# Kernel tuning notes

Measured on AMD Instinct MI355X. Metric: run time of the kernel, lower is better.

Reference implementation:

```python
import jax, jax.numpy as jnp
import numpy as np

B_, T_, DX_, DZ_ = 64, 1024, 64, 1024


def setup_inputs() -> dict:
    key = jax.random.key(0)
    k1, k2, k3, k4, k5 = jax.random.split(key, 5)
    x = jax.random.normal(k1, (B_, T_, DX_), dtype=jnp.float32)
    # obs_model weight (nn.Linear(d_z, d_x).weight): shape (d_x, d_z)
    Bw = jax.random.normal(k2, (DX_, DZ_), dtype=jnp.float32) / np.sqrt(DZ_).astype(np.float32)
    # nn.RNN params (uniform +-1/sqrt(d_z) like torch init)
    bound = 1.0 / np.sqrt(DZ_).astype(np.float32)
    W_hh = jax.random.uniform(k3, (DZ_, DZ_), dtype=jnp.float32, minval=-bound, maxval=bound)
    b_ih = jax.random.uniform(k4, (DZ_,), dtype=jnp.float32, minval=-bound, maxval=bound)
    b_hh = jax.random.uniform(k5, (DZ_,), dtype=jnp.float32, minval=-bound, maxval=bound)
    return {"x": x, "Bw": Bw, "W_hh": W_hh, "b_ih": b_ih, "b_hh": b_hh, "n": 64}


def reference(x, Bw, W_hh, b_ih, b_hh, n):
    # x: (b, T, d_x); Bw: (d_x, d_z); W_hh: (d_z, d_z)
    b, T, dx = x.shape
    pinvB = jnp.linalg.pinv(Bw)                      # (d_z, d_x)
    # candidate reset states z_t = (pinv(B) @ x[:, t].T).T for all t
    zx = jnp.einsum('btx,zx->btz', x, pinvB)         # (b, T, d_z)
    # reset at t == 0 (initial h) and every t % n == 0 (t != 0 case coincides
    # with t == 0 where h is already zx[:, 0], so a single mask is exact)
    reset = (jnp.arange(T) % n) == 0                 # (T,) bool
    bias = b_ih + b_hh                               # input is zero: W_ih @ 0 drops out

    def step(h, inputs):
        m, zr = inputs                               # m: scalar bool, zr: (b, d_z)
        h_in = jnp.where(m, zr, h)
        out = jnp.tanh(h_in @ W_hh.T + bias)         # vanilla tanh RNN cell, zero input
        return out, out

    zr_seq = jnp.swapaxes(zx, 0, 1)                  # (T, b, d_z)
    _, zs = jax.lax.scan(step, zx[:, 0], (reset, zr_seq))
    return jnp.swapaxes(zs, 0, 1)                    # (b, T, d_z)
```

## Files before the change

### kernel.cpp

```cpp
#include <hip/hip_runtime.h>
#include <cstdint>
#include <cstddef>

typedef __attribute__((ext_vector_type(8))) __bf16 bf16x8;
typedef __attribute__((ext_vector_type(4))) float  f32x4;

static_assert(sizeof(bf16x8) == 16, "bf16x8 must be 16B");

__device__ __forceinline__ float fast_tanh(float x) {
    float e = __expf(2.0f * x);
    return 1.0f - 2.0f * __builtin_amdgcn_rcpf(e + 1.0f);
}

__device__ __forceinline__ bf16x8 load_h(const __bf16* p) {
    union { bf16x8 v; unsigned long long q[2]; } u;
    unsigned long long* qp = (unsigned long long*)p;
    u.q[0] = __hip_atomic_load(qp, __ATOMIC_RELAXED, __HIP_MEMORY_SCOPE_AGENT);
    u.q[1] = __hip_atomic_load(qp + 1, __ATOMIC_RELAXED, __HIP_MEMORY_SCOPE_AGENT);
    return u.v;
}

__global__ void k_bias(const float* __restrict__ b_ih, const float* __restrict__ b_hh,
                       float* __restrict__ bias, int* __restrict__ cnt) {
    int i = blockIdx.x * 256 + threadIdx.x;
    bias[i] = b_ih[i] + b_hh[i];
    if (blockIdx.x == 0) cnt[threadIdx.x] = 0;
}

__global__ void k_shufw(const float* __restrict__ W, __bf16* __restrict__ Ws) {
    int id = blockIdx.x * 256 + threadIdx.x;
    int t = id >> 11;
    int c = (id >> 6) & 31;
    int L = id & 63;
    const float* src = W + (size_t)(t * 16 + (L & 15)) * 1024 + c * 32 + (L >> 4) * 8;
    __bf16* dst = Ws + (size_t)id * 8;
#pragma unroll
    for (int j = 0; j < 8; ++j) dst[j] = (__bf16)src[j];
}

__global__ void k_gram(const float* __restrict__ Bw, float* __restrict__ M) {
    int i = blockIdx.x;
    int j = threadIdx.x >> 2;
    int q = threadIdx.x & 3;
    const float4* a = (const float4*)(Bw + (size_t)i * 1024) + q * 64;
    const float4* b = (const float4*)(Bw + (size_t)j * 1024) + q * 64;
    float acc = 0.f;
#pragma unroll 8
    for (int t = 0; t < 64; ++t) {
        float4 av = a[t], bv = b[t];
        acc += av.x * bv.x + av.y * bv.y + av.z * bv.z + av.w * bv.w;
    }
    acc += __shfl_xor(acc, 1);
    acc += __shfl_xor(acc, 2);
    if (q == 0) M[i * 64 + j] = acc;
}

__global__ __launch_bounds__(1024) void k_newton(const float* __restrict__ M,
                                                 float* __restrict__ Minv) {
    __shared__ float Mm[4096];
    __shared__ float X[4096];
    __shared__ float Tt[4096];
    const int tid = threadIdx.x;
    const int i = tid & 63;
    const int w = tid >> 6;
    for (int p = tid; p < 4096; p += 1024) {
        Mm[p] = M[p];
        int r = p >> 6, c2 = p & 63;
        X[p] = (r == c2) ? 0.941f : 0.0f;
    }
    __syncthreads();
    for (int it = 0; it < 6; ++it) {
        float r[4] = {0.f, 0.f, 0.f, 0.f};
        for (int kk = 0; kk < 64; ++kk) {
            float mv = Mm[(kk << 6) + i];
            float4 x4 = *(const float4*)&X[(kk << 6) + (w << 2)];
            r[0] += mv * x4.x; r[1] += mv * x4.y; r[2] += mv * x4.z; r[3] += mv * x4.w;
        }
#pragma unroll
        for (int jj = 0; jj < 4; ++jj) Tt[(((w << 2) + jj) << 6) + i] = r[jj];
        __syncthreads();
        float r2[4];
#pragma unroll
        for (int jj = 0; jj < 4; ++jj) r2[jj] = 2.f * X[(((w << 2) + jj) << 6) + i];
        for (int kq = 0; kq < 16; ++kq) {
            float xv0 = X[((kq * 4 + 0) << 6) + i];
            float xv1 = X[((kq * 4 + 1) << 6) + i];
            float xv2 = X[((kq * 4 + 2) << 6) + i];
            float xv3 = X[((kq * 4 + 3) << 6) + i];
#pragma unroll
            for (int jj = 0; jj < 4; ++jj) {
                float4 t4 = *(const float4*)&Tt[(((w << 2) + jj) << 6) + (kq << 2)];
                r2[jj] -= xv0 * t4.x + xv1 * t4.y + xv2 * t4.z + xv3 * t4.w;
            }
        }
        __syncthreads();
#pragma unroll
        for (int jj = 0; jj < 4; ++jj) X[(((w << 2) + jj) << 6) + i] = r2[jj];
        __syncthreads();
    }
    for (int p = tid; p < 4096; p += 1024) Minv[p] = X[p];
}

__global__ void k_t1(const float* __restrict__ x, const float* __restrict__ Minv,
                     float* __restrict__ T1) {
    int id = blockIdx.x * 256 + threadIdx.x;
    int r = id >> 6, xp = id & 63;
    const float* xr = x + ((size_t)(r >> 4) * 1024 + (size_t)(r & 15) * 64) * 64;
    const float* mr = Minv + (size_t)xp * 64;
    float acc = 0.f;
    for (int t = 0; t < 64; ++t) acc += xr[t] * mr[t];
    T1[id] = acc;
}

__global__ void k_h0(const float* __restrict__ T1, const float* __restrict__ Bw,
                     __bf16* __restrict__ H0) {
    int r = blockIdx.y;
    int z = blockIdx.x * 256 + threadIdx.x;
    const float* t1 = T1 + (size_t)r * 64;
    float acc = 0.f;
    for (int xp = 0; xp < 64; ++xp) acc += t1[xp] * Bw[(size_t)xp * 1024 + z];
    H0[(size_t)r * 1024 + z] = (__bf16)acc;
}

__global__ __launch_bounds__(256) void k_step(
    const __bf16* __restrict__ Hin, const __bf16* __restrict__ Ws,
    const float* __restrict__ bias, __bf16* __restrict__ Hout,
    float* __restrict__ out, int kstep) {
    const int tid = threadIdx.x;
    const int w = tid >> 6;
    const int lane = tid & 63;
    const int row = lane & 15;
    const int quad = lane >> 4;
    const int bm = blockIdx.x, bn = blockIdx.y;

    const __bf16* Arow = Hin + (size_t)(bm * 64 + w * 16 + row) * 1024 + quad * 8;
    const __bf16* B0 = Ws + ((size_t)((bn * 2 + 0) * 32) * 64 + lane) * 8;
    const __bf16* B1 = Ws + ((size_t)((bn * 2 + 1) * 32) * 64 + lane) * 8;

    f32x4 acc0 = {0.f, 0.f, 0.f, 0.f};
    f32x4 acc1 = {0.f, 0.f, 0.f, 0.f};
#pragma unroll 8
    for (int c = 0; c < 32; ++c) {
        bf16x8 a = *(const bf16x8*)(Arow + c * 32);
        bf16x8 b0 = *(const bf16x8*)(B0 + (size_t)c * 512);
        bf16x8 b1 = *(const bf16x8*)(B1 + (size_t)c * 512);
        acc0 = __builtin_amdgcn_mfma_f32_16x16x32_bf16(a, b0, acc0, 0, 0, 0);
        acc1 = __builtin_amdgcn_mfma_f32_16x16x32_bf16(a, b1, acc1, 0, 0, 0);
    }
#pragma unroll
    for (int nt = 0; nt < 2; ++nt) {
        const f32x4 acc = nt ? acc1 : acc0;
        const int col = bn * 32 + nt * 16 + row;
        const float bv = bias[col];
#pragma unroll
        for (int i = 0; i < 4; ++i) {
            const int m = bm * 64 + w * 16 + quad * 4 + i;
            float v = tanhf(acc[i] + bv);
            const int b_ = m >> 4, s_ = m & 15;
            out[((size_t)b_ * 1024 + (size_t)s_ * 64 + kstep) * 1024 + col] = v;
            Hout[(size_t)m * 1024 + col] = (__bf16)v;
        }
    }
}

__global__ __launch_bounds__(256, 1) void k_persist(
    const __bf16* __restrict__ Ws, const float* __restrict__ bias,
    __bf16* __restrict__ H0, __bf16* __restrict__ H1,
    float* __restrict__ out, int* cnt) {
    __shared__ __bf16 Bs[65536];
    const int tid = threadIdx.x;
    const int bid = blockIdx.x;
    const int bm = bid & 15;
    const int bn = bid >> 4;
    const int lane = tid & 63;
    const int w = tid >> 6;
    const int row = lane & 15, quad = lane >> 4;

    {
        const bf16x8* src = (const bf16x8*)(Ws + ((size_t)bn << 16));
        bf16x8* dst = (bf16x8*)Bs;
#pragma unroll
        for (int it = 0; it < 32; ++it) dst[it * 256 + tid] = src[it * 256 + tid];
    }
    float bv[4];
#pragma unroll
    for (int nt = 0; nt < 4; ++nt) bv[nt] = bias[bn * 64 + nt * 16 + row];
    __syncthreads();

    const size_t aoff = (size_t)(bm * 64 + w * 16 + row) * 1024 + quad * 8;
    int* mycnt = cnt + bm * 16;

    for (int k = 0; k < 64; ++k) {
        const __bf16* Hin = (k & 1) ? H1 : H0;
        __bf16* Hout = (k & 1) ? H0 : H1;
        const __bf16* A = Hin + aoff;
        const bf16x8* Bl = (const bf16x8*)Bs + lane;

        f32x4 acc0 = {0.f, 0.f, 0.f, 0.f};
        f32x4 acc1 = acc0, acc2 = acc0, acc3 = acc0;

        bf16x8 a0 = load_h(A + 0 * 32), a1 = load_h(A + 1 * 32),
               a2 = load_h(A + 2 * 32), a3 = load_h(A + 3 * 32),
               a4 = load_h(A + 4 * 32), a5 = load_h(A + 5 * 32),
               a6 = load_h(A + 6 * 32), a7 = load_h(A + 7 * 32);

#define KSTEP(AA, CC)                                                                     \
        acc0 = __builtin_amdgcn_mfma_f32_16x16x32_bf16(AA, Bl[(0 * 32 + (CC)) * 64], acc0, 0, 0, 0); \
        acc1 = __builtin_amdgcn_mfma_f32_16x16x32_bf16(AA, Bl[(1 * 32 + (CC)) * 64], acc1, 0, 0, 0); \
        acc2 = __builtin_amdgcn_mfma_f32_16x16x32_bf16(AA, Bl[(2 * 32 + (CC)) * 64], acc2, 0, 0, 0); \
        acc3 = __builtin_amdgcn_mfma_f32_16x16x32_bf16(AA, Bl[(3 * 32 + (CC)) * 64], acc3, 0, 0, 0);

        for (int c = 0; c < 24; c += 8) {
            bf16x8 n0 = load_h(A + (c + 8) * 32),  n1 = load_h(A + (c + 9) * 32),
                   n2 = load_h(A + (c + 10) * 32), n3 = load_h(A + (c + 11) * 32),
                   n4 = load_h(A + (c + 12) * 32), n5 = load_h(A + (c + 13) * 32),
                   n6 = load_h(A + (c + 14) * 32), n7 = load_h(A + (c + 15) * 32);
            KSTEP(a0, c + 0) KSTEP(a1, c + 1) KSTEP(a2, c + 2) KSTEP(a3, c + 3)
            KSTEP(a4, c + 4) KSTEP(a5, c + 5) KSTEP(a6, c + 6) KSTEP(a7, c + 7)
            a0 = n0; a1 = n1; a2 = n2; a3 = n3; a4 = n4; a5 = n5; a6 = n6; a7 = n7;
        }
        KSTEP(a0, 24) KSTEP(a1, 25) KSTEP(a2, 26) KSTEP(a3, 27)
        KSTEP(a4, 28) KSTEP(a5, 29) KSTEP(a6, 30) KSTEP(a7, 31)
#undef KSTEP

        const int mbase = bm * 64 + w * 16 + quad * 4;
#pragma unroll
        for (int nt = 0; nt < 4; ++nt) {
            const f32x4 acc = nt == 0 ? acc0 : nt == 1 ? acc1 : nt == 2 ? acc2 : acc3;
            const int col = bn * 64 + nt * 16 + row;
            const float bb = bv[nt];
#pragma unroll
            for (int i2 = 0; i2 < 4; ++i2) {
                const int m = mbase + i2;
                const float v = fast_tanh(acc[i2] + bb);
                const int b_ = m >> 4, s_ = m & 15;
                out[((size_t)b_ * 1024 + (size_t)s_ * 64 + k) * 1024 + col] = v;
                if (k < 63) {
                    union { __bf16 h; unsigned short s; } cv;
                    cv.h = (__bf16)v;
                    __hip_atomic_store((unsigned short*)(Hout + (size_t)m * 1024 + col),
                                       cv.s, __ATOMIC_RELAXED, __HIP_MEMORY_SCOPE_AGENT);
                }
            }
        }

        __syncthreads();
        if (k < 63) {
            if (tid == 0) {
                __hip_atomic_fetch_add(mycnt, 1, __ATOMIC_RELAXED, __HIP_MEMORY_SCOPE_AGENT);
                const int target = (k + 1) * 16;
                while (__hip_atomic_load(mycnt, __ATOMIC_RELAXED, __HIP_MEMORY_SCOPE_AGENT) < target)
                    __builtin_amdgcn_s_sleep(1);
            }
            __syncthreads();
        }
    }
}

extern "C" void kernel_launch(void* const* d_in, const int* in_sizes, int n_in,
                              void* d_out, int out_size, void* d_ws, size_t ws_size,
                              hipStream_t stream) {
    const float* x = (const float*)d_in[0];
    const float* Bw = (const float*)d_in[1];
    const float* W_hh = (const float*)d_in[2];
    const float* b_ih = (const float*)d_in[3];
    const float* b_hh = (const float*)d_in[4];
    float* out = (float*)d_out;
    uint8_t* ws = (uint8_t*)d_ws;

    __bf16* Ws = (__bf16*)(ws);
    __bf16* H0 = (__bf16*)(ws + (2ull << 20));
    __bf16* H1 = (__bf16*)(ws + (4ull << 20));
    float* bias = (float*)(ws + (6ull << 20));
    float* Mg = (float*)(ws + (6ull << 20) + 4096);
    float* Minv = (float*)(ws + (6ull << 20) + 20480);
    float* T1 = (float*)(ws + (6ull << 20) + 36864);
    int* cnt = (int*)(ws + (6ull << 20) + 36864 + 262144);

    hipLaunchKernelGGL(k_bias, dim3(4), dim3(256), 0, stream, b_ih, b_hh, bias, cnt);
    hipLaunchKernelGGL(k_shufw, dim3(512), dim3(256), 0, stream, W_hh, Ws);
    hipLaunchKernelGGL(k_gram, dim3(64), dim3(256), 0, stream, Bw, Mg);
    hipLaunchKernelGGL(k_newton, dim3(1), dim3(1024), 0, stream, Mg, Minv);
    hipLaunchKernelGGL(k_t1, dim3(256), dim3(256), 0, stream, x, Minv, T1);
    hipLaunchKernelGGL(k_h0, dim3(4, 1024), dim3(256), 0, stream, T1, Bw, H0);

    const __bf16* Wsp = Ws;
    const float* biasp = bias;
    __bf16* h0p = H0;
    __bf16* h1p = H1;
    float* outp = out;
    int* cntp = cnt;
    void* kargs[] = {&Wsp, &biasp, &h0p, &h1p, &outp, &cntp};
    hipError_t err = hipLaunchCooperativeKernel((void*)k_persist, dim3(256), dim3(256),
                                                kargs, 0, stream);
    if (err != hipSuccess) {
        __bf16* bufs[2] = {H0, H1};
        for (int k = 0; k < 64; ++k) {
            hipLaunchKernelGGL(k_step, dim3(16, 32), dim3(256), 0, stream,
                               bufs[k & 1], Ws, bias, bufs[(k + 1) & 1], out, k);
        }
    }
}
```

Baseline: 913.6 us.

## Stage persistent-kernel outputs through LDS for vectorized stores after the barrier

The persistent recurrence kernel now writes tanh results into a padded shared-memory tile, then reads them back so each thread owns 16 contiguous columns of one row. The bf16 hidden-state handoff becomes four 64-bit atomic stores instead of scalar 16-bit atomics. The fp32 output is written with nontemporal 16-byte stores issued after the inter-block barrier, so it overlaps the next step instead of delaying the handoff. All 32 A fragments are also loaded up front. This costs an extra LDS round trip and barrier per step, more registers, and 17 KB more shared memory.

```diff
diff --git a/kernel.cpp b/kernel.cpp
--- a/kernel.cpp
+++ b/kernel.cpp
@@ -6,18 +6,11 @@
 typedef __attribute__((ext_vector_type(4))) float  f32x4;
 
 static_assert(sizeof(bf16x8) == 16, "bf16x8 must be 16B");
+static_assert(sizeof(f32x4) == 16, "f32x4 must be 16B");
 
 __device__ __forceinline__ float fast_tanh(float x) {
     float e = __expf(2.0f * x);
     return 1.0f - 2.0f * __builtin_amdgcn_rcpf(e + 1.0f);
-}
-
-__device__ __forceinline__ bf16x8 load_h(const __bf16* p) {
-    union { bf16x8 v; unsigned long long q[2]; } u;
-    unsigned long long* qp = (unsigned long long*)p;
-    u.q[0] = __hip_atomic_load(qp, __ATOMIC_RELAXED, __HIP_MEMORY_SCOPE_AGENT);
-    u.q[1] = __hip_atomic_load(qp + 1, __ATOMIC_RELAXED, __HIP_MEMORY_SCOPE_AGENT);
-    return u.v;
 }
 
 __global__ void k_bias(const float* __restrict__ b_ih, const float* __restrict__ b_hh,
@@ -168,13 +161,13 @@
     __bf16* __restrict__ H0, __bf16* __restrict__ H1,
     float* __restrict__ out, int* cnt) {
     __shared__ __bf16 Bs[65536];
+    __shared__ float oT[64 * 68];
     const int tid = threadIdx.x;
-    const int bid = blockIdx.x;
-    const int bm = bid & 15;
-    const int bn = bid >> 4;
     const int lane = tid & 63;
     const int w = tid >> 6;
     const int row = lane & 15, quad = lane >> 4;
+    const int bm = blockIdx.x & 15;
+    const int bn = blockIdx.x >> 4;
 
     {
         const bf16x8* src = (const bf16x8*)(Ws + ((size_t)bn << 16));
@@ -188,72 +181,90 @@
     __syncthreads();
 
     const size_t aoff = (size_t)(bm * 64 + w * 16 + row) * 1024 + quad * 8;
-    int* mycnt = cnt + bm * 16;
+    int* gcnt = cnt + bm * 16;
+    const bf16x8* Bl = (const bf16x8*)Bs + lane;
+
+    const int tr = tid >> 2;
+    const int tc = (tid & 3) << 4;
+    const int gm = bm * 64 + tr;
+    float* outp = out + ((size_t)(gm >> 4) * 1024 + (size_t)(gm & 15) * 64) * 1024
+                      + (size_t)bn * 64 + tc;
+    const size_t hoff = (size_t)gm * 1024 + (size_t)(bn * 64 + tc);
 
     for (int k = 0; k < 64; ++k) {
         const __bf16* Hin = (k & 1) ? H1 : H0;
         __bf16* Hout = (k & 1) ? H0 : H1;
-        const __bf16* A = Hin + aoff;
-        const bf16x8* Bl = (const bf16x8*)Bs + lane;
+        const unsigned long long* Aq = (const unsigned long long*)(Hin + aoff);
+
+        bf16x8 av[32];
+#pragma unroll
+        for (int c = 0; c < 32; ++c) {
+            union { bf16x8 v; unsigned long long q[2]; } u;
+            u.q[0] = __hip_atomic_load(Aq + c * 8,     __ATOMIC_RELAXED,
+                                       __HIP_MEMORY_SCOPE_AGENT);
+            u.q[1] = __hip_atomic_load(Aq + c * 8 + 1, __ATOMIC_RELAXED,
+                                       __HIP_MEMORY_SCOPE_AGENT);
+            av[c] = u.v;
+        }
 
         f32x4 acc0 = {0.f, 0.f, 0.f, 0.f};
         f32x4 acc1 = acc0, acc2 = acc0, acc3 = acc0;
-
-        bf16x8 a0 = load_h(A + 0 * 32), a1 = load_h(A + 1 * 32),
-               a2 = load_h(A + 2 * 32), a3 = load_h(A + 3 * 32),
-               a4 = load_h(A + 4 * 32), a5 = load_h(A + 5 * 32),
-               a6 = load_h(A + 6 * 32), a7 = load_h(A + 7 * 32);
-
-#define KSTEP(AA, CC)                                                                     \
-        acc0 = __builtin_amdgcn_mfma_f32_16x16x32_bf16(AA, Bl[(0 * 32 + (CC)) * 64], acc0, 0, 0, 0); \
-        acc1 = __builtin_amdgcn_mfma_f32_16x16x32_bf16(AA, Bl[(1 * 32 + (CC)) * 64], acc1, 0, 0, 0); \
-        acc2 = __builtin_amdgcn_mfma_f32_16x16x32_bf16(AA, Bl[(2 * 32 + (CC)) * 64], acc2, 0, 0, 0); \
-        acc3 = __builtin_amdgcn_mfma_f32_16x16x32_bf16(AA, Bl[(3 * 32 + (CC)) * 64], acc3, 0, 0, 0);
-
-        for (int c = 0; c < 24; c += 8) {
-            bf16x8 n0 = load_h(A + (c + 8) * 32),  n1 = load_h(A + (c + 9) * 32),
-                   n2 = load_h(A + (c + 10) * 32), n3 = load_h(A + (c + 11) * 32),
-                   n4 = load_h(A + (c + 12) * 32), n5 = load_h(A + (c + 13) * 32),
-                   n6 = load_h(A + (c + 14) * 32), n7 = load_h(A + (c + 15) * 32);
-            KSTEP(a0, c + 0) KSTEP(a1, c + 1) KSTEP(a2, c + 2) KSTEP(a3, c + 3)
-            KSTEP(a4, c + 4) KSTEP(a5, c + 5) KSTEP(a6, c + 6) KSTEP(a7, c + 7)
-            a0 = n0; a1 = n1; a2 = n2; a3 = n3; a4 = n4; a5 = n5; a6 = n6; a7 = n7;
-        }
-        KSTEP(a0, 24) KSTEP(a1, 25) KSTEP(a2, 26) KSTEP(a3, 27)
-        KSTEP(a4, 28) KSTEP(a5, 29) KSTEP(a6, 30) KSTEP(a7, 31)
-#undef KSTEP
-
-        const int mbase = bm * 64 + w * 16 + quad * 4;
+#pragma unroll
+        for (int c = 0; c < 32; ++c) {
+            acc0 = __builtin_amdgcn_mfma_f32_16x16x32_bf16(av[c], Bl[(0 * 32 + c) * 64], acc0, 0, 0, 0);
+            acc1 = __builtin_amdgcn_mfma_f32_16x16x32_bf16(av[c], Bl[(1 * 32 + c) * 64], acc1, 0, 0, 0);
+            acc2 = __builtin_amdgcn_mfma_f32_16x16x32_bf16(av[c], Bl[(2 * 32 + c) * 64], acc2, 0, 0, 0);
+            acc3 = __builtin_amdgcn_mfma_f32_16x16x32_bf16(av[c], Bl[(3 * 32 + c) * 64], acc3, 0, 0, 0);
+        }
+
 #pragma unroll
         for (int nt = 0; nt < 4; ++nt) {
             const f32x4 acc = nt == 0 ? acc0 : nt == 1 ? acc1 : nt == 2 ? acc2 : acc3;
-            const int col = bn * 64 + nt * 16 + row;
-            const float bb = bv[nt];
 #pragma unroll
             for (int i2 = 0; i2 < 4; ++i2) {
-                const int m = mbase + i2;
-                const float v = fast_tanh(acc[i2] + bb);
-                const int b_ = m >> 4, s_ = m & 15;
-                out[((size_t)b_ * 1024 + (size_t)s_ * 64 + k) * 1024 + col] = v;
-                if (k < 63) {
-                    union { __bf16 h; unsigned short s; } cv;
-                    cv.h = (__bf16)v;
-                    __hip_atomic_store((unsigned short*)(Hout + (size_t)m * 1024 + col),
-                                       cv.s, __ATOMIC_RELAXED, __HIP_MEMORY_SCOPE_AGENT);
-                }
+                const int r = w * 16 + quad * 4 + i2;
+                oT[r * 68 + nt * 16 + row] = fast_tanh(acc[i2] + bv[nt]);
             }
         }
-
+        __syncthreads();
+
+        const f32x4 o0 = *(const f32x4*)&oT[tr * 68 + tc + 0];
+        const f32x4 o1 = *(const f32x4*)&oT[tr * 68 + tc + 4];
+        const f32x4 o2 = *(const f32x4*)&oT[tr * 68 + tc + 8];
+        const f32x4 o3 = *(const f32x4*)&oT[tr * 68 + tc + 12];
+
+        if (k < 63) {
+            union { __bf16 h[16]; unsigned long long q[4]; } hp;
+#pragma unroll
+            for (int j = 0; j < 4; ++j) {
+                hp.h[0 + j] = (__bf16)o0[j];
+                hp.h[4 + j] = (__bf16)o1[j];
+                hp.h[8 + j] = (__bf16)o2[j];
+                hp.h[12 + j] = (__bf16)o3[j];
+            }
+            unsigned long long* hq = (unsigned long long*)(Hout + hoff);
+#pragma unroll
+            for (int j = 0; j < 4; ++j)
+                __hip_atomic_store(hq + j, hp.q[j], __ATOMIC_RELAXED,
+                                   __HIP_MEMORY_SCOPE_AGENT);
+        }
         __syncthreads();
         if (k < 63) {
             if (tid == 0) {
-                __hip_atomic_fetch_add(mycnt, 1, __ATOMIC_RELAXED, __HIP_MEMORY_SCOPE_AGENT);
+                __hip_atomic_fetch_add(gcnt, 1, __ATOMIC_RELAXED,
+                                       __HIP_MEMORY_SCOPE_AGENT);
                 const int target = (k + 1) * 16;
-                while (__hip_atomic_load(mycnt, __ATOMIC_RELAXED, __HIP_MEMORY_SCOPE_AGENT) < target)
+                while (__hip_atomic_load(gcnt, __ATOMIC_RELAXED,
+                                         __HIP_MEMORY_SCOPE_AGENT) < target)
                     __builtin_amdgcn_s_sleep(1);
             }
             __syncthreads();
         }
+        float* op = outp + (size_t)k * 1024;
+        __builtin_nontemporal_store(o0, (f32x4*)(op + 0));
+        __builtin_nontemporal_store(o1, (f32x4*)(op + 4));
+        __builtin_nontemporal_store(o2, (f32x4*)(op + 8));
+        __builtin_nontemporal_store(o3, (f32x4*)(op + 12));
     }
 }
 
```

New measurement: 1.253 ms. 37.1% more time.
